# Kernel tuning notes

Measured on AMD Instinct MI355X. Metric: run time of the kernel, lower is better.

## Reference

```python
import jax, jax.numpy as jnp
import numpy as np

NEG_SLOPE = 0.2


def gat_layer(x, src, dst, W, att_src, att_dst, bias, concat):
    # x: [N, Fin]; W: [Fin, H*C]; att_*: [H, C]; bias: [H*C] or [C]
    n = x.shape[0]
    H, C = att_src.shape
    h = (x @ W).reshape(n, H, C)                      # [N,H,C]
    a_src = jnp.einsum('nhc,hc->nh', h, att_src)      # [N,H]
    a_dst = jnp.einsum('nhc,hc->nh', h, att_dst)      # [N,H]
    e = a_src[src] + a_dst[dst]                       # [E,H]
    e = jnp.where(e > 0, e, NEG_SLOPE * e)            # leaky_relu(0.2)
    # segment softmax over edges grouped by destination node
    m = jax.ops.segment_max(e, dst, num_segments=n)   # [N,H]
    m = jnp.where(jnp.isfinite(m), m, 0.0)            # empty segments
    ex = jnp.exp(e - m[dst])                          # [E,H]
    s = jax.ops.segment_sum(ex, dst, num_segments=n)  # [N,H]
    alpha = ex / (s[dst] + 1e-16)                     # [E,H]
    msg = h[src] * alpha[..., None]                   # [E,H,C]
    out = jax.ops.segment_sum(msg, dst, num_segments=n)  # [N,H,C]
    out = out.reshape(n, H * C) if concat else out.mean(axis=1)
    return out + bias


def setup_inputs() -> dict:
    key = jax.random.key(0)
    ks = jax.random.split(key, 10)
    N, E, FIN, HID, HEADS, OUT = 50000, 800000, 128, 64, 4, 16
    x = jax.random.normal(ks[0], (N, FIN), dtype=jnp.float32)
    edge_index = jax.random.randint(ks[1], (2, E), 0, N, dtype=jnp.int32)
    sc = 0.05
    return {
        'x': x,
        'edge_index': edge_index,
        'W1': jax.random.normal(ks[2], (FIN, HEADS * HID), jnp.float32) * sc,
        'att_src1': jax.random.normal(ks[3], (HEADS, HID), jnp.float32) * sc,
        'att_dst1': jax.random.normal(ks[4], (HEADS, HID), jnp.float32) * sc,
        'b1': jnp.zeros((HEADS * HID,), jnp.float32),
        'W2': jax.random.normal(ks[5], (HEADS * HID, OUT), jnp.float32) * sc,
        'att_src2': jax.random.normal(ks[6], (1, OUT), jnp.float32) * sc,
        'att_dst2': jax.random.normal(ks[7], (1, OUT), jnp.float32) * sc,
        'b2': jnp.zeros((OUT,), jnp.float32),
    }


def reference(x, edge_index, W1, att_src1, att_dst1, b1, W2, att_src2, att_dst2, b2):
    src, dst = edge_index[0], edge_index[1]
    h = gat_layer(x, src, dst, W1, att_src1, att_dst1, b1, concat=True)
    h = jax.nn.relu(h)
    # dropout is identity in eval mode
    out = gat_layer(h, src, dst, W2, att_src2, att_dst2, b2, concat=False)
    return out
```

## Files before the change

### kernel.cpp

```cpp
#include <hip/hip_runtime.h>
#include <hip/hip_bf16.h>

#define FIN 128
#define HC 256
#define H1 4
#define C1 64
#define OUT2 16

typedef __attribute__((ext_vector_type(8))) short bf16x8;
typedef __attribute__((ext_vector_type(4))) float f32x4;

__device__ inline float bf2f(unsigned short u) {
    union { unsigned int i; float f; } v; v.i = ((unsigned int)u) << 16; return v.f;
}
__device__ inline unsigned short f2bf(float f) {
    union { float f; unsigned int i; } v; v.f = f;
    unsigned int i = v.i;
    return (unsigned short)((i + 0x7FFFu + ((i >> 16) & 1u)) >> 16);
}
__device__ inline unsigned int pack2(float a, float b) {
    return (unsigned int)f2bf(a) | ((unsigned int)f2bf(b) << 16);
}

__global__ __launch_bounds__(256) void w1t_kernel(
    const float* __restrict__ W1, unsigned short* __restrict__ W1t)
{
    int t = blockIdx.x * 256 + threadIdx.x;
    if (t >= HC * FIN) return;
    int c = t >> 7, k = t & 127;
    W1t[t] = f2bf(W1[k * HC + c]);
}

__global__ __launch_bounds__(256) void gemm1_mfma_kernel(
    const float* __restrict__ x, const unsigned short* __restrict__ W1t,
    unsigned short* __restrict__ h1, int N)
{
    const int t  = threadIdx.x;
    const int wv = t >> 6;
    const int l  = t & 63;
    const int c0 = l & 15;
    const int h  = l >> 4;
    const int R0 = blockIdx.x * 64 + wv * 16;

    f32x4 acc[16];
    #pragma unroll
    for (int j = 0; j < 16; j++) acc[j] = (f32x4){0.f, 0.f, 0.f, 0.f};

    int arow = R0 + c0;
    if (arow > N - 1) arow = N - 1;
    const float* xrow = x + (size_t)arow * FIN;

    for (int kb = 0; kb < FIN; kb += 32) {
        float4 f0 = *(const float4*)&xrow[kb + 8 * h];
        float4 f1 = *(const float4*)&xrow[kb + 8 * h + 4];
        union { bf16x8 v; unsigned int u[4]; } af;
        af.u[0] = pack2(f0.x, f0.y);
        af.u[1] = pack2(f0.z, f0.w);
        af.u[2] = pack2(f1.x, f1.y);
        af.u[3] = pack2(f1.z, f1.w);
        #pragma unroll
        for (int j = 0; j < 16; j++) {
            int col = 16 * j + c0;
            union { bf16x8 v; uint4 u; } bf;
            bf.u = *(const uint4*)&W1t[(size_t)col * FIN + kb + 8 * h];
            acc[j] = __builtin_amdgcn_mfma_f32_16x16x32_bf16(af.v, bf.v, acc[j], 0, 0, 0);
        }
    }

    #pragma unroll
    for (int r = 0; r < 4; r++) {
        int row = R0 + 4 * h + r;
        if (row < N) {
            unsigned short* hp = &h1[(size_t)row * HC + c0];
            #pragma unroll
            for (int j = 0; j < 16; j++)
                hp[16 * j] = f2bf(acc[j][r]);
        }
    }
}

__global__ __launch_bounds__(256) void attdots1_kernel(
    const unsigned short* __restrict__ h1, const float* __restrict__ att_src,
    const float* __restrict__ att_dst, float* __restrict__ a_src,
    float* __restrict__ a_dst, int N)
{
    int wave = (int)((blockIdx.x * blockDim.x + threadIdx.x) >> 6);
    int l = threadIdx.x & 63;
    if (wave >= N) return;
    int h = l >> 4;
    int ci = 4 * (l & 15);
    uint2 hv = *(const uint2*)&h1[(size_t)wave * HC + 4*l];
    float f0 = bf2f((unsigned short)(hv.x & 0xffff));
    float f1 = bf2f((unsigned short)(hv.x >> 16));
    float f2 = bf2f((unsigned short)(hv.y & 0xffff));
    float f3 = bf2f((unsigned short)(hv.y >> 16));
    float4 asv = *(const float4*)&att_src[h * C1 + ci];
    float4 adv = *(const float4*)&att_dst[h * C1 + ci];
    float ps = f0*asv.x + f1*asv.y + f2*asv.z + f3*asv.w;
    float pd = f0*adv.x + f1*adv.y + f2*adv.z + f3*adv.w;
    #pragma unroll
    for (int off = 1; off < 16; off <<= 1) {
        ps += __shfl_xor(ps, off, 64);
        pd += __shfl_xor(pd, off, 64);
    }
    if ((l & 15) == 0) {
        a_src[wave * 4 + h] = ps;
        a_dst[wave * 4 + h] = pd;
    }
}

__global__ __launch_bounds__(256) void count_kernel(
    const int* __restrict__ dst, int* __restrict__ counts, int E)
{
    int e = blockIdx.x * blockDim.x + threadIdx.x;
    if (e < E) atomicAdd(&counts[dst[e]], 1);
}

__global__ __launch_bounds__(1024) void scan1_kernel(
    const int* __restrict__ counts, int* __restrict__ rowptr,
    int* __restrict__ bsum, int n)
{
    __shared__ int sm[1024];
    int tid = threadIdx.x;
    int i = blockIdx.x * 1024 + tid;
    int v = (i < n) ? counts[i] : 0;
    sm[tid] = v;
    __syncthreads();
    for (int off = 1; off < 1024; off <<= 1) {
        int tv = (tid >= off) ? sm[tid - off] : 0;
        __syncthreads();
        sm[tid] += tv;
        __syncthreads();
    }
    if (i < n) rowptr[i] = sm[tid] - v;
    if (tid == 1023) bsum[blockIdx.x] = sm[1023];
}

__global__ __launch_bounds__(1024) void scan2_kernel(
    int* __restrict__ bsum, int* __restrict__ rowptr, int nb, int N, int E)
{
    __shared__ int sm[1024];
    int tid = threadIdx.x;
    int v = (tid < nb) ? bsum[tid] : 0;
    sm[tid] = v;
    __syncthreads();
    for (int off = 1; off < 1024; off <<= 1) {
        int tv = (tid >= off) ? sm[tid - off] : 0;
        __syncthreads();
        sm[tid] += tv;
        __syncthreads();
    }
    if (tid < nb) bsum[tid] = sm[tid] - v;
    if (tid == 0) rowptr[N] = E;
}

__global__ __launch_bounds__(1024) void scan3_kernel(
    int* __restrict__ rowptr, const int* __restrict__ bsum, int n)
{
    int i = blockIdx.x * 1024 + threadIdx.x;
    if (i < n) rowptr[i] += bsum[blockIdx.x];
}

__global__ __launch_bounds__(256) void scatter_kernel(
    const int* __restrict__ src, const int* __restrict__ dst,
    const int* __restrict__ rowptr, int* __restrict__ cursor,
    const float* __restrict__ a_src, const float* __restrict__ a_dst,
    uint4* __restrict__ csr_rec, int E)
{
    int e = blockIdx.x * blockDim.x + threadIdx.x;
    if (e >= E) return;
    int s = src[e], d = dst[e];
    int pos = rowptr[d] + atomicAdd(&cursor[d], 1);
    float4 av = *(const float4*)&a_src[(size_t)s * 4];
    float4 bv = *(const float4*)&a_dst[(size_t)d * 4];
    float w0, w1, w2, w3, v;
    v = av.x + bv.x; v = v > 0.f ? v : 0.2f * v; w0 = __expf(v);
    v = av.y + bv.y; v = v > 0.f ? v : 0.2f * v; w1 = __expf(v);
    v = av.z + bv.z; v = v > 0.f ? v : 0.2f * v; w2 = __expf(v);
    v = av.w + bv.w; v = v > 0.f ? v : 0.2f * v; w3 = __expf(v);
    uint4 rec;
    rec.x = (unsigned int)s;
    rec.y = (unsigned int)d;
    rec.z = pack2(w0, w1);
    rec.w = pack2(w2, w3);
    csr_rec[pos] = rec;
}

__global__ __launch_bounds__(256) void agg1_kernel(
    const unsigned short* __restrict__ h1,
    const uint4* __restrict__ csr_rec, const int* __restrict__ rowptr,
    const float* __restrict__ b1, unsigned short* __restrict__ out1, int N)
{
    int wave = (int)((blockIdx.x * blockDim.x + threadIdx.x) >> 6);
    if (wave >= N) return;
    int node = __builtin_amdgcn_readfirstlane(wave);
    int l = threadIdx.x & 63;
    int h = l >> 4;
    int rs = rowptr[node], re = rowptr[node + 1];
    float a0 = 0.f, a1 = 0.f, a2 = 0.f, a3 = 0.f, sw = 0.f;
    int p = rs;
    for (; p + 8 <= re; p += 8) {
        uint4 r[8];
        #pragma unroll
        for (int j = 0; j < 8; j++) r[j] = csr_rec[p + j];
        uint2 hv[8];
        #pragma unroll
        for (int j = 0; j < 8; j++)
            hv[j] = *(const uint2*)&h1[(size_t)(int)r[j].x * HC + 4 * l];
        #pragma unroll
        for (int j = 0; j < 8; j++) {
            unsigned int wsel = (h & 2) ? r[j].w : r[j].z;
            float wv = bf2f((unsigned short)((h & 1) ? (wsel >> 16) : (wsel & 0xffff)));
            a0 = fmaf(wv, bf2f((unsigned short)(hv[j].x & 0xffff)), a0);
            a1 = fmaf(wv, bf2f((unsigned short)(hv[j].x >> 16)), a1);
            a2 = fmaf(wv, bf2f((unsigned short)(hv[j].y & 0xffff)), a2);
            a3 = fmaf(wv, bf2f((unsigned short)(hv[j].y >> 16)), a3);
            sw += wv;
        }
    }
    for (; p < re; p++) {
        uint4 r = csr_rec[p];
        uint2 hv = *(const uint2*)&h1[(size_t)(int)r.x * HC + 4 * l];
        unsigned int wsel = (h & 2) ? r.w : r.z;
        float wv = bf2f((unsigned short)((h & 1) ? (wsel >> 16) : (wsel & 0xffff)));
        a0 = fmaf(wv, bf2f((unsigned short)(hv.x & 0xffff)), a0);
        a1 = fmaf(wv, bf2f((unsigned short)(hv.x >> 16)), a1);
        a2 = fmaf(wv, bf2f((unsigned short)(hv.y & 0xffff)), a2);
        a3 = fmaf(wv, bf2f((unsigned short)(hv.y >> 16)), a3);
        sw += wv;
    }
    float inv = 1.f / (sw + 1e-16f);
    float4 bv = *(const float4*)&b1[4 * l];
    float o0 = fmaxf(a0 * inv + bv.x, 0.f);
    float o1 = fmaxf(a1 * inv + bv.y, 0.f);
    float o2 = fmaxf(a2 * inv + bv.z, 0.f);
    float o3 = fmaxf(a3 * inv + bv.w, 0.f);
    unsigned int* op = (unsigned int*)&out1[(size_t)node * HC + 4 * l];
    op[0] = pack2(o0, o1);
    op[1] = pack2(o2, o3);
}

__global__ __launch_bounds__(256) void gemm2_kernel(
    const unsigned short* __restrict__ out1, const float* __restrict__ W2,
    const float* __restrict__ att_src2, const float* __restrict__ att_dst2,
    float* __restrict__ h2, float* __restrict__ a_src2, float* __restrict__ a_dst2,
    int N)
{
    __shared__ float xs[16][260];
    __shared__ float W2s[256 * 16];
    int t = threadIdx.x;
    int rb = blockIdx.x * 16;
    {
        int r = t >> 4;
        int k0 = (t & 15) * 4;
        int gr = rb + r;
        #pragma unroll
        for (int j = 0; j < 4; j++) {
            uint2 v = make_uint2(0, 0);
            if (gr < N) v = *(const uint2*)&out1[(size_t)gr * HC + k0 + 64*j];
            xs[r][k0 + 64*j + 0] = bf2f((unsigned short)(v.x & 0xffff));
            xs[r][k0 + 64*j + 1] = bf2f((unsigned short)(v.x >> 16));
            xs[r][k0 + 64*j + 2] = bf2f((unsigned short)(v.y & 0xffff));
            xs[r][k0 + 64*j + 3] = bf2f((unsigned short)(v.y >> 16));
        }
    }
    {
        #pragma unroll
        for (int j = 0; j < 4; j++) {
            float4 v = ((const float4*)W2)[j * 256 + t];
            ((float4*)W2s)[j * 256 + t] = v;
        }
    }
    __syncthreads();
    int r = t >> 4, c = t & 15;
    float acc = 0.f;
    #pragma unroll 8
    for (int k = 0; k < 256; k++)
        acc = fmaf(xs[r][k], W2s[k * 16 + c], acc);
    int gr = rb + r;
    float ps = acc * att_src2[c];
    float pd = acc * att_dst2[c];
    #pragma unroll
    for (int off = 1; off < 16; off <<= 1) {
        ps += __shfl_xor(ps, off, 64);
        pd += __shfl_xor(pd, off, 64);
    }
    if (gr < N) {
        h2[(size_t)gr * OUT2 + c] = acc;
        if (c == 0) { a_src2[gr] = ps; a_dst2[gr] = pd; }
    }
}

__global__ __launch_bounds__(256) void w2csr_kernel(
    const uint4* __restrict__ csr_rec,
    const float* __restrict__ a_src2, const float* __restrict__ a_dst2,
    float* __restrict__ w2csr, int E)
{
    int p = blockIdx.x * blockDim.x + threadIdx.x;
    if (p >= E) return;
    uint4 r = csr_rec[p];
    float v = a_src2[(int)r.x] + a_dst2[(int)r.y];
    v = v > 0.f ? v : 0.2f * v;
    w2csr[p] = __expf(v);
}

__global__ __launch_bounds__(256) void agg2_kernel(
    const float* __restrict__ h2,
    const int* __restrict__ csr_rec_i, const float* __restrict__ w2csr,
    const int* __restrict__ rowptr,
    const float* __restrict__ b2, float* __restrict__ out, int N)
{
    int wave = (int)((blockIdx.x * blockDim.x + threadIdx.x) >> 6);
    if (wave >= N) return;
    int node = __builtin_amdgcn_readfirstlane(wave);
    int l = threadIdx.x & 63;
    int g = l >> 4, c = l & 15;
    int rs = rowptr[node], re = rowptr[node + 1];
    float acc = 0.f, sw = 0.f;
    int p = rs + g;
    for (; p + 4 < re; p += 8) {
        int sn0 = csr_rec_i[(size_t)p * 4];
        int sn1 = csr_rec_i[(size_t)(p + 4) * 4];
        float w0 = w2csr[p];
        float w1 = w2csr[p + 4];
        float x0 = h2[(size_t)sn0 * OUT2 + c];
        float x1 = h2[(size_t)sn1 * OUT2 + c];
        acc = fmaf(w0, x0, acc);
        acc = fmaf(w1, x1, acc);
        sw += w0 + w1;
    }
    if (p < re) {
        int sn = csr_rec_i[(size_t)p * 4];
        float w0 = w2csr[p];
        acc = fmaf(w0, h2[(size_t)sn * OUT2 + c], acc);
        sw += w0;
    }
    acc += __shfl_xor(acc, 16, 64);
    acc += __shfl_xor(acc, 32, 64);
    sw += __shfl_xor(sw, 16, 64);
    sw += __shfl_xor(sw, 32, 64);
    if (l < 16)
        out[(size_t)node * OUT2 + l] = acc / (sw + 1e-16f) + b2[l];
}

extern "C" void kernel_launch(void* const* d_in, const int* in_sizes, int n_in,
                              void* d_out, int out_size, void* d_ws, size_t ws_size,
                              hipStream_t stream)
{
    const float* x        = (const float*)d_in[0];
    const int*   ei       = (const int*)d_in[1];
    const float* W1       = (const float*)d_in[2];
    const float* att_src1 = (const float*)d_in[3];
    const float* att_dst1 = (const float*)d_in[4];
    const float* b1       = (const float*)d_in[5];
    const float* W2       = (const float*)d_in[6];
    const float* att_src2 = (const float*)d_in[7];
    const float* att_dst2 = (const float*)d_in[8];
    const float* b2       = (const float*)d_in[9];
    float* out = (float*)d_out;

    const int N = in_sizes[0] / FIN;
    const int E = in_sizes[1] / 2;
    const int* srcv = ei;
    const int* dstv = ei + E;

    char* base = (char*)d_ws;
    #define ALLOC(ptr, type, nelem) \
        type* ptr = (type*)base; base += (((size_t)(nelem) * sizeof(type) + 255) & ~(size_t)255);
    ALLOC(h1,      unsigned short, (size_t)N * HC)
    ALLOC(out1,    unsigned short, (size_t)N * HC)
    ALLOC(csr_rec, uint4,          (size_t)E)
    ALLOC(h2,      float,          (size_t)N * OUT2)
    ALLOC(a_src1v, float,          (size_t)N * 4)
    ALLOC(a_dst1v, float,          (size_t)N * 4)
    ALLOC(a_src2v, float,          (size_t)N)
    ALLOC(a_dst2v, float,          (size_t)N)
    ALLOC(counts,  int,            (size_t)2 * N)
    ALLOC(w2csr,   float,          (size_t)E)
    ALLOC(rowptr,  int,            (size_t)N + 1)
    ALLOC(bsum,    int,            1024)
    #undef ALLOC
    int* cursor = counts + N;
    unsigned short* W1t = (unsigned short*)csr_rec;

    const int nb = (N + 1023) / 1024;

    (void)hipMemsetAsync(counts, 0, sizeof(int) * 2 * (size_t)N, stream);

    w1t_kernel<<<(HC * FIN + 255) / 256, 256, 0, stream>>>(W1, W1t);
    gemm1_mfma_kernel<<<(N + 63) / 64, 256, 0, stream>>>(x, W1t, h1, N);
    attdots1_kernel<<<(N + 3) / 4, 256, 0, stream>>>(h1, att_src1, att_dst1, a_src1v, a_dst1v, N);
    count_kernel<<<(E + 255) / 256, 256, 0, stream>>>(dstv, counts, E);
    scan1_kernel<<<nb, 1024, 0, stream>>>(counts, rowptr, bsum, N);
    scan2_kernel<<<1, 1024, 0, stream>>>(bsum, rowptr, nb, N, E);
    scan3_kernel<<<nb, 1024, 0, stream>>>(rowptr, bsum, N);
    scatter_kernel<<<(E + 255) / 256, 256, 0, stream>>>(srcv, dstv, rowptr, cursor,
                                                        a_src1v, a_dst1v, csr_rec, E);
    agg1_kernel<<<(N + 3) / 4, 256, 0, stream>>>(h1, csr_rec, rowptr, b1, out1, N);
    gemm2_kernel<<<(N + 15) / 16, 256, 0, stream>>>(out1, W2, att_src2, att_dst2, h2, a_src2v, a_dst2v, N);
    w2csr_kernel<<<(E + 255) / 256, 256, 0, stream>>>(csr_rec, a_src2v, a_dst2v, w2csr, E);
    agg2_kernel<<<(N + 3) / 4, 256, 0, stream>>>(h2, (const int*)csr_rec, w2csr, rowptr, b2, out, N);
}
```

Baseline: 253.4 us.

## Fuse attention dots, second GEMM and edge weights into neighboring kernels

Merges the W1 transpose with edge counting into one prep kernel. It computes layer-1 attention dots from the MFMA accumulators inside gemm1, and folds the 256x16 second-layer GEMM plus its attention dots into agg1 as a per-wave reduction. Edge weights for layer 2 are now recomputed inside agg2, so the out1 and w2csr buffers and four launches disappear. The cost is a heavy 16-value, 6-step shuffle reduction per node in agg1, extra register pressure in gemm1, and per-edge exp recomputation in agg2.

```diff
diff --git a/kernel.cpp b/kernel.cpp
--- a/kernel.cpp
+++ b/kernel.cpp
@@ -22,18 +22,26 @@
     return (unsigned int)f2bf(a) | ((unsigned int)f2bf(b) << 16);
 }
 
-__global__ __launch_bounds__(256) void w1t_kernel(
-    const float* __restrict__ W1, unsigned short* __restrict__ W1t)
-{
-    int t = blockIdx.x * 256 + threadIdx.x;
-    if (t >= HC * FIN) return;
-    int c = t >> 7, k = t & 127;
-    W1t[t] = f2bf(W1[k * HC + c]);
+__global__ __launch_bounds__(256) void prep_kernel(
+    const float* __restrict__ W1, unsigned short* __restrict__ W1t,
+    const int* __restrict__ dst, int* __restrict__ counts, int E)
+{
+    int b = blockIdx.x;
+    if (b < 128) {
+        int t = b * 256 + threadIdx.x;
+        int c = t >> 7, k = t & 127;
+        W1t[t] = f2bf(W1[k * HC + c]);
+    } else {
+        int e = (b - 128) * 256 + threadIdx.x;
+        if (e < E) atomicAdd(&counts[dst[e]], 1);
+    }
 }
 
 __global__ __launch_bounds__(256) void gemm1_mfma_kernel(
     const float* __restrict__ x, const unsigned short* __restrict__ W1t,
-    unsigned short* __restrict__ h1, int N)
+    const float* __restrict__ att_src, const float* __restrict__ att_dst,
+    unsigned short* __restrict__ h1, float* __restrict__ a_src,
+    float* __restrict__ a_dst, int N)
 {
     const int t  = threadIdx.x;
     const int wv = t >> 6;
@@ -67,6 +75,55 @@
         }
     }
 
+    float avs[16], avd[16];
+    #pragma unroll
+    for (int j = 0; j < 16; j++) {
+        avs[j] = att_src[16 * j + c0];
+        avd[j] = att_dst[16 * j + c0];
+    }
+    f32x4 ps[4], pd[4];
+    #pragma unroll
+    for (int hd = 0; hd < 4; hd++) {
+        ps[hd] = (f32x4){0.f, 0.f, 0.f, 0.f};
+        pd[hd] = (f32x4){0.f, 0.f, 0.f, 0.f};
+        #pragma unroll
+        for (int jj = 0; jj < 4; jj++) {
+            int j = 4 * hd + jj;
+            #pragma unroll
+            for (int r = 0; r < 4; r++) {
+                ps[hd][r] = fmaf(acc[j][r], avs[j], ps[hd][r]);
+                pd[hd][r] = fmaf(acc[j][r], avd[j], pd[hd][r]);
+            }
+        }
+    }
+    #pragma unroll
+    for (int hd = 0; hd < 4; hd++)
+        #pragma unroll
+        for (int r = 0; r < 4; r++) {
+            float s = ps[hd][r], d = pd[hd][r];
+            s += __shfl_xor(s, 1, 64);  d += __shfl_xor(d, 1, 64);
+            s += __shfl_xor(s, 2, 64);  d += __shfl_xor(d, 2, 64);
+            s += __shfl_xor(s, 4, 64);  d += __shfl_xor(d, 4, 64);
+            s += __shfl_xor(s, 8, 64);  d += __shfl_xor(d, 8, 64);
+            ps[hd][r] = s;  pd[hd][r] = d;
+        }
+    {
+        float s_sel = 0.f, d_sel = 0.f;
+        #pragma unroll
+        for (int hd = 0; hd < 4; hd++)
+            #pragma unroll
+            for (int r = 0; r < 4; r++) {
+                bool m = (c0 == hd * 4 + r);
+                s_sel = m ? ps[hd][r] : s_sel;
+                d_sel = m ? pd[hd][r] : d_sel;
+            }
+        int row = R0 + 4 * h + (c0 & 3);
+        if (row < N) {
+            a_src[row * 4 + (c0 >> 2)] = s_sel;
+            a_dst[row * 4 + (c0 >> 2)] = d_sel;
+        }
+    }
+
     #pragma unroll
     for (int r = 0; r < 4; r++) {
         int row = R0 + 4 * h + r;
@@ -77,43 +134,6 @@
                 hp[16 * j] = f2bf(acc[j][r]);
         }
     }
-}
-
-__global__ __launch_bounds__(256) void attdots1_kernel(
-    const unsigned short* __restrict__ h1, const float* __restrict__ att_src,
-    const float* __restrict__ att_dst, float* __restrict__ a_src,
-    float* __restrict__ a_dst, int N)
-{
-    int wave = (int)((blockIdx.x * blockDim.x + threadIdx.x) >> 6);
-    int l = threadIdx.x & 63;
-    if (wave >= N) return;
-    int h = l >> 4;
-    int ci = 4 * (l & 15);
-    uint2 hv = *(const uint2*)&h1[(size_t)wave * HC + 4*l];
-    float f0 = bf2f((unsigned short)(hv.x & 0xffff));
-    float f1 = bf2f((unsigned short)(hv.x >> 16));
-    float f2 = bf2f((unsigned short)(hv.y & 0xffff));
-    float f3 = bf2f((unsigned short)(hv.y >> 16));
-    float4 asv = *(const float4*)&att_src[h * C1 + ci];
-    float4 adv = *(const float4*)&att_dst[h * C1 + ci];
-    float ps = f0*asv.x + f1*asv.y + f2*asv.z + f3*asv.w;
-    float pd = f0*adv.x + f1*adv.y + f2*adv.z + f3*adv.w;
-    #pragma unroll
-    for (int off = 1; off < 16; off <<= 1) {
-        ps += __shfl_xor(ps, off, 64);
-        pd += __shfl_xor(pd, off, 64);
-    }
-    if ((l & 15) == 0) {
-        a_src[wave * 4 + h] = ps;
-        a_dst[wave * 4 + h] = pd;
-    }
-}
-
-__global__ __launch_bounds__(256) void count_kernel(
-    const int* __restrict__ dst, int* __restrict__ counts, int E)
-{
-    int e = blockIdx.x * blockDim.x + threadIdx.x;
-    if (e < E) atomicAdd(&counts[dst[e]], 1);
 }
 
 __global__ __launch_bounds__(1024) void scan1_kernel(
@@ -189,7 +209,10 @@
 __global__ __launch_bounds__(256) void agg1_kernel(
     const unsigned short* __restrict__ h1,
     const uint4* __restrict__ csr_rec, const int* __restrict__ rowptr,
-    const float* __restrict__ b1, unsigned short* __restrict__ out1, int N)
+    const float* __restrict__ b1, const float* __restrict__ W2,
+    const float* __restrict__ att_src2, const float* __restrict__ att_dst2,
+    float* __restrict__ h2, float* __restrict__ a_src2, float* __restrict__ a_dst2,
+    int N)
 {
     int wave = (int)((blockIdx.x * blockDim.x + threadIdx.x) >> 6);
     if (wave >= N) return;
@@ -231,82 +254,60 @@
     }
     float inv = 1.f / (sw + 1e-16f);
     float4 bv = *(const float4*)&b1[4 * l];
-    float o0 = fmaxf(a0 * inv + bv.x, 0.f);
-    float o1 = fmaxf(a1 * inv + bv.y, 0.f);
-    float o2 = fmaxf(a2 * inv + bv.z, 0.f);
-    float o3 = fmaxf(a3 * inv + bv.w, 0.f);
-    unsigned int* op = (unsigned int*)&out1[(size_t)node * HC + 4 * l];
-    op[0] = pack2(o0, o1);
-    op[1] = pack2(o2, o3);
-}
-
-__global__ __launch_bounds__(256) void gemm2_kernel(
-    const unsigned short* __restrict__ out1, const float* __restrict__ W2,
-    const float* __restrict__ att_src2, const float* __restrict__ att_dst2,
-    float* __restrict__ h2, float* __restrict__ a_src2, float* __restrict__ a_dst2,
-    int N)
-{
-    __shared__ float xs[16][260];
-    __shared__ float W2s[256 * 16];
-    int t = threadIdx.x;
-    int rb = blockIdx.x * 16;
+    float o[4];
+    o[0] = fmaxf(a0 * inv + bv.x, 0.f);
+    o[1] = fmaxf(a1 * inv + bv.y, 0.f);
+    o[2] = fmaxf(a2 * inv + bv.z, 0.f);
+    o[3] = fmaxf(a3 * inv + bv.w, 0.f);
+
+    float part[16];
+    #pragma unroll
+    for (int j = 0; j < 16; j++) part[j] = 0.f;
+    #pragma unroll
+    for (int i = 0; i < 4; i++) {
+        const float4* wrow = (const float4*)&W2[(size_t)(4 * l + i) * OUT2];
+        float4 wa = wrow[0], wb = wrow[1], wc = wrow[2], wd = wrow[3];
+        part[0]  = fmaf(o[i], wa.x, part[0]);  part[1]  = fmaf(o[i], wa.y, part[1]);
+        part[2]  = fmaf(o[i], wa.z, part[2]);  part[3]  = fmaf(o[i], wa.w, part[3]);
+        part[4]  = fmaf(o[i], wb.x, part[4]);  part[5]  = fmaf(o[i], wb.y, part[5]);
+        part[6]  = fmaf(o[i], wb.z, part[6]);  part[7]  = fmaf(o[i], wb.w, part[7]);
+        part[8]  = fmaf(o[i], wc.x, part[8]);  part[9]  = fmaf(o[i], wc.y, part[9]);
+        part[10] = fmaf(o[i], wc.z, part[10]); part[11] = fmaf(o[i], wc.w, part[11]);
+        part[12] = fmaf(o[i], wd.x, part[12]); part[13] = fmaf(o[i], wd.y, part[13]);
+        part[14] = fmaf(o[i], wd.z, part[14]); part[15] = fmaf(o[i], wd.w, part[15]);
+    }
+    #pragma unroll
+    for (int off = 1; off < 64; off <<= 1)
+        #pragma unroll
+        for (int j = 0; j < 16; j++)
+            part[j] += __shfl_xor(part[j], off, 64);
+
     {
-        int r = t >> 4;
-        int k0 = (t & 15) * 4;
-        int gr = rb + r;
-        #pragma unroll
-        for (int j = 0; j < 4; j++) {
-            uint2 v = make_uint2(0, 0);
-            if (gr < N) v = *(const uint2*)&out1[(size_t)gr * HC + k0 + 64*j];
-            xs[r][k0 + 64*j + 0] = bf2f((unsigned short)(v.x & 0xffff));
-            xs[r][k0 + 64*j + 1] = bf2f((unsigned short)(v.x >> 16));
-            xs[r][k0 + 64*j + 2] = bf2f((unsigned short)(v.y & 0xffff));
-            xs[r][k0 + 64*j + 3] = bf2f((unsigned short)(v.y >> 16));
-        }
-    }
-    {
-        #pragma unroll
-        for (int j = 0; j < 4; j++) {
-            float4 v = ((const float4*)W2)[j * 256 + t];
-            ((float4*)W2s)[j * 256 + t] = v;
-        }
-    }
-    __syncthreads();
-    int r = t >> 4, c = t & 15;
-    float acc = 0.f;
-    #pragma unroll 8
-    for (int k = 0; k < 256; k++)
-        acc = fmaf(xs[r][k], W2s[k * 16 + c], acc);
-    int gr = rb + r;
-    float ps = acc * att_src2[c];
-    float pd = acc * att_dst2[c];
-    #pragma unroll
-    for (int off = 1; off < 16; off <<= 1) {
-        ps += __shfl_xor(ps, off, 64);
-        pd += __shfl_xor(pd, off, 64);
-    }
-    if (gr < N) {
-        h2[(size_t)gr * OUT2 + c] = acc;
-        if (c == 0) { a_src2[gr] = ps; a_dst2[gr] = pd; }
-    }
-}
-
-__global__ __launch_bounds__(256) void w2csr_kernel(
-    const uint4* __restrict__ csr_rec,
-    const float* __restrict__ a_src2, const float* __restrict__ a_dst2,
-    float* __restrict__ w2csr, int E)
-{
-    int p = blockIdx.x * blockDim.x + threadIdx.x;
-    if (p >= E) return;
-    uint4 r = csr_rec[p];
-    float v = a_src2[(int)r.x] + a_dst2[(int)r.y];
-    v = v > 0.f ? v : 0.2f * v;
-    w2csr[p] = __expf(v);
+        float ps = 0.f, pdv = 0.f;
+        const float4* s4 = (const float4*)att_src2;
+        const float4* d4 = (const float4*)att_dst2;
+        #pragma unroll
+        for (int q = 0; q < 4; q++) {
+            float4 sv = s4[q], dv = d4[q];
+            ps  = fmaf(part[4*q+0], sv.x, ps);  pdv = fmaf(part[4*q+0], dv.x, pdv);
+            ps  = fmaf(part[4*q+1], sv.y, ps);  pdv = fmaf(part[4*q+1], dv.y, pdv);
+            ps  = fmaf(part[4*q+2], sv.z, ps);  pdv = fmaf(part[4*q+2], dv.z, pdv);
+            ps  = fmaf(part[4*q+3], sv.w, ps);  pdv = fmaf(part[4*q+3], dv.w, pdv);
+        }
+        if (l == 0) { a_src2[node] = ps; a_dst2[node] = pdv; }
+    }
+    if (l < 16) {
+        float v = 0.f;
+        #pragma unroll
+        for (int j = 0; j < 16; j++) v = (l == j) ? part[j] : v;
+        h2[(size_t)node * OUT2 + l] = v;
+    }
 }
 
 __global__ __launch_bounds__(256) void agg2_kernel(
     const float* __restrict__ h2,
-    const int* __restrict__ csr_rec_i, const float* __restrict__ w2csr,
+    const int* __restrict__ csr_rec_i,
+    const float* __restrict__ a_src2, const float* __restrict__ a_dst2,
     const int* __restrict__ rowptr,
     const float* __restrict__ b2, float* __restrict__ out, int N)
 {
@@ -316,22 +317,29 @@
     int l = threadIdx.x & 63;
     int g = l >> 4, c = l & 15;
     int rs = rowptr[node], re = rowptr[node + 1];
+    float ad = a_dst2[node];
     float acc = 0.f, sw = 0.f;
     int p = rs + g;
     for (; p + 4 < re; p += 8) {
         int sn0 = csr_rec_i[(size_t)p * 4];
         int sn1 = csr_rec_i[(size_t)(p + 4) * 4];
-        float w0 = w2csr[p];
-        float w1 = w2csr[p + 4];
+        float e0 = a_src2[sn0] + ad;
+        float e1 = a_src2[sn1] + ad;
         float x0 = h2[(size_t)sn0 * OUT2 + c];
         float x1 = h2[(size_t)sn1 * OUT2 + c];
+        e0 = e0 > 0.f ? e0 : 0.2f * e0;
+        e1 = e1 > 0.f ? e1 : 0.2f * e1;
+        float w0 = __expf(e0);
+        float w1 = __expf(e1);
         acc = fmaf(w0, x0, acc);
         acc = fmaf(w1, x1, acc);
         sw += w0 + w1;
     }
     if (p < re) {
         int sn = csr_rec_i[(size_t)p * 4];
-        float w0 = w2csr[p];
+        float e0 = a_src2[sn] + ad;
+        e0 = e0 > 0.f ? e0 : 0.2f * e0;
+        float w0 = __expf(e0);
         acc = fmaf(w0, h2[(size_t)sn * OUT2 + c], acc);
         sw += w0;
     }
@@ -368,7 +376,6 @@
     #define ALLOC(ptr, type, nelem) \
         type* ptr = (type*)base; base += (((size_t)(nelem) * sizeof(type) + 255) & ~(size_t)255);
     ALLOC(h1,      unsigned short, (size_t)N * HC)
-    ALLOC(out1,    unsigned short, (size_t)N * HC)
     ALLOC(csr_rec, uint4,          (size_t)E)
     ALLOC(h2,      float,          (size_t)N * OUT2)
     ALLOC(a_src1v, float,          (size_t)N * 4)
@@ -376,7 +383,6 @@
     ALLOC(a_src2v, float,          (size_t)N)
     ALLOC(a_dst2v, float,          (size_t)N)
     ALLOC(counts,  int,            (size_t)2 * N)
-    ALLOC(w2csr,   float,          (size_t)E)
     ALLOC(rowptr,  int,            (size_t)N + 1)
     ALLOC(bsum,    int,            1024)
     #undef ALLOC
@@ -387,17 +393,17 @@
 
     (void)hipMemsetAsync(counts, 0, sizeof(int) * 2 * (size_t)N, stream);
 
-    w1t_kernel<<<(HC * FIN + 255) / 256, 256, 0, stream>>>(W1, W1t);
-    gemm1_mfma_kernel<<<(N + 63) / 64, 256, 0, stream>>>(x, W1t, h1, N);
-    attdots1_kernel<<<(N + 3) / 4, 256, 0, stream>>>(h1, att_src1, att_dst1, a_src1v, a_dst1v, N);
-    count_kernel<<<(E + 255) / 256, 256, 0, stream>>>(dstv, counts, E);
+    prep_kernel<<<128 + (E + 255) / 256, 256, 0, stream>>>(W1, W1t, dstv, counts, E);
+    gemm1_mfma_kernel<<<(N + 63) / 64, 256, 0, stream>>>(x, W1t, att_src1, att_dst1,
+                                                         h1, a_src1v, a_dst1v, N);
     scan1_kernel<<<nb, 1024, 0, stream>>>(counts, rowptr, bsum, N);
     scan2_kernel<<<1, 1024, 0, stream>>>(bsum, rowptr, nb, N, E);
     scan3_kernel<<<nb, 1024, 0, stream>>>(rowptr, bsum, N);
     scatter_kernel<<<(E + 255) / 256, 256, 0, stream>>>(srcv, dstv, rowptr, cursor,
                                                         a_src1v, a_dst1v, csr_rec, E);
-    agg1_kernel<<<(N + 3) / 4, 256, 0, stream>>>(h1, csr_rec, rowptr, b1, out1, N);
-    gemm2_kernel<<<(N + 15) / 16, 256, 0, stream>>>(out1, W2, att_src2, att_dst2, h2, a_src2v, a_dst2v, N);
-    w2csr_kernel<<<(E + 255) / 256, 256, 0, stream>>>(csr_rec, a_src2v, a_dst2v, w2csr, E);
-    agg2_kernel<<<(N + 3) / 4, 256, 0, stream>>>(h2, (const int*)csr_rec, w2csr, rowptr, b2, out, N);
-}
+    agg1_kernel<<<(N + 3) / 4, 256, 0, stream>>>(h1, csr_rec, rowptr, b1, W2,
+                                                 att_src2, att_dst2,
+                                                 h2, a_src2v, a_dst2v, N);
+    agg2_kernel<<<(N + 3) / 4, 256, 0, stream>>>(h2, (const int*)csr_rec,
+                                                 a_src2v, a_dst2v, rowptr, b2, out, N);
+}
```

Measured after the change: 277.4 us. 9.5% more time.
